# Optimization experiments

Hardware: AMD Instinct MI355X
Metric: run time of the kernel (lower is better)

Reference implementation:

```python
import jax, jax.numpy as jnp
import numpy as np

HIDDEN = 300
INPUT_DIM = 300


def setup_inputs() -> dict:
    key = jax.random.key(0)
    k_in, k_wih, k_whh, k_bih, k_bhh = jax.random.split(key, 5)
    bound = 1.0 / np.sqrt(HIDDEN)  # PyTorch RNNCell init: U(-1/sqrt(H), 1/sqrt(H))
    inputs = jax.random.normal(k_in, (512, 512, INPUT_DIM), dtype=jnp.float32)
    W_ih = jax.random.uniform(k_wih, (HIDDEN, INPUT_DIM), jnp.float32, -bound, bound)
    W_hh = jax.random.uniform(k_whh, (HIDDEN, HIDDEN), jnp.float32, -bound, bound)
    b_ih = jax.random.uniform(k_bih, (HIDDEN,), jnp.float32, -bound, bound)
    b_hh = jax.random.uniform(k_bhh, (HIDDEN,), jnp.float32, -bound, bound)
    return {"inputs": inputs, "W_ih": W_ih, "W_hh": W_hh, "b_ih": b_ih, "b_hh": b_hh}


def reference(inputs, W_ih, W_hh, b_ih, b_hh):
    # inputs: [seq, batch, input_dim]; vanilla tanh RNNCell scanned over time.
    seq, bz, _ = inputs.shape
    # Precompute input projections for all timesteps in one big GEMM.
    x_proj = jnp.einsum('sbi,hi->sbh', inputs, W_ih) + b_ih + b_hh  # [seq, batch, H]

    def step(ht, xp):
        ht = jnp.tanh(xp + ht @ W_hh.T)
        return ht, None

    h0 = jnp.zeros((bz, HIDDEN), dtype=inputs.dtype)
    ht, _ = jax.lax.scan(step, h0, x_proj)
    return ht
```

## Files before the change

### kernel.cpp

```cpp
#include <hip/hip_runtime.h>
#include <hip/hip_bf16.h>


typedef unsigned short u16;
typedef unsigned int   u32;
typedef __attribute__((ext_vector_type(8)))  short bf16x8;
typedef __attribute__((ext_vector_type(4)))  short s16x4;
typedef __attribute__((ext_vector_type(4)))  float f32x4;
typedef __attribute__((ext_vector_type(16))) float f32x16;
typedef __attribute__((ext_vector_type(2)))  unsigned int u32x2;
typedef __attribute__((ext_vector_type(4)))  unsigned int u32x4;

#define HID 300
#define KP  320
#define SEQ 512
#define BZ  512
#define MTOT (SEQ*BZ)

__device__ __forceinline__ u16 f2bf(float f) {
    u32 u = __float_as_uint(f);
    return (u16)((u + 0x7FFFu + ((u >> 16) & 1u)) >> 16);
}
__device__ __forceinline__ float bf2f(u16 h) {
    return __uint_as_float((u32)h << 16);
}
__device__ __forceinline__ float tanh_fast(float x) {
    float e = __builtin_amdgcn_exp2f(x * 2.8853900817779268f);
    float r = __builtin_amdgcn_rcpf(e + 1.0f);
    return __builtin_fmaf(-2.0f, r, 1.0f);
}
__device__ __forceinline__ u32 pack2(float a, float b) {
    __hip_bfloat162 t = __float22bfloat162_rn(float2{a, b});
    return *(u32*)&t;
}
__device__ __forceinline__ void lds_barrier() {
    asm volatile("s_waitcnt lgkmcnt(0)\n\ts_barrier" ::: "memory");
}

__global__ void prep_kernel(const float* __restrict__ wih,
                            const float* __restrict__ whh,
                            const float* __restrict__ bih,
                            const float* __restrict__ bhh,
                            u16* __restrict__ wihp, u16* __restrict__ whhp,
                            float* __restrict__ bias) {
    int n = blockIdx.x, k = threadIdx.x;
    bool v = (n < HID) && (k < HID);
    int src = n * HID + k, dst = n * KP + k;
    wihp[dst] = v ? f2bf(wih[src]) : (u16)0;
    whhp[dst] = v ? f2bf(whh[src]) : (u16)0;
    if (k == 0) bias[n] = (n < HID) ? (bih[n] + bhh[n]) : 0.0f;
}

__global__ __launch_bounds__(512, 1) void xproj_kernel(
    const float* __restrict__ in, const u16* __restrict__ wihp,
    const float* __restrict__ bias, u16* __restrict__ xp) {
    __shared__ __align__(16) u16 As[2][4096];
    __shared__ __align__(16) u16 Bs[3][10240];

    const int tid = threadIdx.x;
    const int w = tid >> 6, l = tid & 63;
    const int mi = w & 3, ni = w >> 2;
    const int l31 = l & 31, l5 = l >> 5;
    const int m0 = blockIdx.x * 128;

    const int sm = tid >> 2, skg = tid & 3;

    f32x16 acc[5];
#pragma unroll
    for (int j = 0; j < 5; ++j)
#pragma unroll
        for (int r = 0; r < 16; ++r) acc[j][r] = 0.0f;

    const f32x4 zf = {0.f, 0.f, 0.f, 0.f};
    auto loadA = [&](int it, f32x4& v0, f32x4& v1) {
        int gk = it * 32 + skg * 8;
        int a0 = gk > 296 ? 296 : gk;
        int a1 = (gk + 4) > 296 ? 296 : (gk + 4);
        const float* p = in + (size_t)(m0 + sm) * HID;
        v0 = *(const f32x4*)(p + a0);
        v1 = *(const f32x4*)(p + a1);
        v0 = (gk > 296) ? zf : v0;
        v1 = ((gk + 4) > 296) ? zf : v1;
    };
    auto writeA = [&](int buf, const f32x4& v0, const f32x4& v1) {
        u32x4 pk;
        pk[0] = pack2(v0[0], v0[1]); pk[1] = pack2(v0[2], v0[3]);
        pk[2] = pack2(v1[0], v1[1]); pk[3] = pack2(v1[2], v1[3]);
        *(u32x4*)&As[buf][(skg >> 1) * 2048 + sm * 16 + (skg & 1) * 8] = pk;
    };
    auto stageB = [&](int buf, int it) {
#pragma unroll
        for (int s = 0; s < 3; ++s) {
            int i = w + 8 * s;
            if (i < 20) {
                int c = i & 3, ng = i >> 2;
                int n = ng * 64 + l;
                const u16* g = wihp + n * KP + it * 32 + c * 8;
                u16* d = &Bs[buf][c * 2560 + ng * 512];
                __builtin_amdgcn_global_load_lds(
                    (const __attribute__((address_space(1))) void*)g,
                    (__attribute__((address_space(3))) void*)d, 16, 0, 0);
            }
        }
    };

    {
        stageB(0, 0);
        f32x4 v0, v1;
        loadA(0, v0, v1);
        writeA(0, v0, v1);
        stageB(1, 1);
        asm volatile("s_waitcnt vmcnt(2)" ::: "memory");
        lds_barrier();
    }

    int cA = 0, cB = 0, sB = 2;
#pragma unroll 1
    for (int it = 0; it < 10; ++it) {
        f32x4 v0, v1;
        if (it < 9) loadA(it + 1, v0, v1);
        if (it < 8) stageB(sB, it + 2);
#pragma unroll
        for (int s = 0; s < 2; ++s) {
            bf16x8 a = *(const bf16x8*)&As[cA][s * 2048 + mi * 512 + l31 * 16 + l5 * 8];
#pragma unroll
            for (int j = 0; j < 5; ++j) {
                bf16x8 b = *(const bf16x8*)&Bs[cB][(s * 2 + l5) * 2560 + ((ni * 5 + j) * 32 + l31) * 8];
                acc[j] = __builtin_amdgcn_mfma_f32_32x32x16_bf16(a, b, acc[j], 0, 0, 0);
            }
        }
        if (it < 9) {
            writeA(cA ^ 1, v0, v1);
            if (it < 8) asm volatile("s_waitcnt vmcnt(3)" ::: "memory");
            else        asm volatile("s_waitcnt vmcnt(2)" ::: "memory");
            lds_barrier();
        }
        cA ^= 1;
        cB = (cB == 2) ? 0 : cB + 1;
        sB = (sB == 2) ? 0 : sB + 1;
    }

    const int mbase = m0 + mi * 32;
#pragma unroll
    for (int j = 0; j < 5; ++j) {
        int n = (ni * 5 + j) * 32 + l31;
        if (n < HID) {
            float bs = bias[n];
#pragma unroll
            for (int reg = 0; reg < 16; ++reg) {
                int row = (reg & 3) + 8 * (reg >> 2) + 4 * l5;
                xp[(size_t)(mbase + row) * HID + n] = f2bf(acc[j][reg] + bs);
            }
        }
    }
}

__global__ __launch_bounds__(512, 2) void rnn_recur_kernel(
    const u16* __restrict__ xp, const u16* __restrict__ whhp,
    float* __restrict__ out) {
    __shared__ __align__(16) u16 hb[2][16 * 328];

    const int tid = threadIdx.x;
    const int w = tid >> 6;
    const int l = tid & 63;
    const int br = l & 15;
    const int q  = l >> 4;
    const int b0 = blockIdx.x * 16;
    const bool t3 = (w < 4);

    for (int i = tid; i < (2 * 16 * 328) / 2; i += 512) ((u32*)hb)[i] = 0;

    bf16x8 Af[3][10];
#pragma unroll
    for (int j = 0; j < 3; ++j) {
        if (j < 2 || t3) {
            const int nt = w + 8 * j;
            const u16* wrow = whhp + (size_t)(nt * 16 + br) * KP;
#pragma unroll
            for (int ks = 0; ks < 10; ++ks)
                Af[j][ks] = *(const bf16x8*)(wrow + ks * 32 + q * 8);
        }
    }
#pragma unroll
    for (int j = 0; j < 3; ++j)
        if (j < 2 || t3)
#pragma unroll
            for (int ks = 0; ks < 10; ++ks)
                asm volatile("" : "+a"(Af[j][ks]));

    int xo[3];
#pragma unroll
    for (int j = 0; j < 3; ++j) {
        int n0 = (w + 8 * j) * 16 + q * 4;
        xo[j] = (n0 < HID && (j < 2 || t3)) ? ((b0 + br) * HID + n0) : -1;
    }

    const s16x4 z4 = {0, 0, 0, 0};
    s16x4 xc[3], xn[3];
#pragma unroll
    for (int j = 0; j < 3; ++j) {
        xc[j] = (xo[j] >= 0) ? *(const s16x4*)(xp + xo[j]) : z4;
        xn[j] = (xo[j] >= 0) ? *(const s16x4*)(xp + (size_t)BZ * HID + xo[j]) : z4;
    }

    lds_barrier();

#pragma unroll 1
    for (int t = 0; t < SEQ; ++t) {
        const u16* hc = hb[t & 1];
        u16*       hn = hb[(t + 1) & 1];

        s16x4 xf[3];
        {
            int t2 = (t + 2 < SEQ) ? (t + 2) : (SEQ - 1);
            const u16* base = xp + (size_t)t2 * (BZ * HID);
#pragma unroll
            for (int j = 0; j < 3; ++j)
                xf[j] = (xo[j] >= 0) ? *(const s16x4*)(base + xo[j]) : z4;
        }

        bf16x8 bL[5];
#pragma unroll
        for (int ks = 0; ks < 5; ++ks)
            bL[ks] = *(const bf16x8*)&hc[br * 328 + ks * 32 + q * 8];

        f32x4 a0L, a1L, a2L;
#pragma unroll
        for (int r = 0; r < 4; ++r) {
            a0L[r] = bf2f((u16)xc[0][r]);
            a1L[r] = bf2f((u16)xc[1][r]);
            a2L[r] = bf2f((u16)xc[2][r]);
        }
#pragma unroll
        for (int ks = 0; ks < 5; ++ks) {
            a0L = __builtin_amdgcn_mfma_f32_16x16x32_bf16(Af[0][ks], bL[ks], a0L, 0, 0, 0);
            a1L = __builtin_amdgcn_mfma_f32_16x16x32_bf16(Af[1][ks], bL[ks], a1L, 0, 0, 0);
            if (t3)
                a2L = __builtin_amdgcn_mfma_f32_16x16x32_bf16(Af[2][ks], bL[ks], a2L, 0, 0, 0);
        }

        bf16x8 bH[5];
#pragma unroll
        for (int ks = 0; ks < 5; ++ks)
            bH[ks] = *(const bf16x8*)&hc[br * 328 + (ks + 5) * 32 + q * 8];

        f32x4 a0H, a1H, a2H;
#pragma unroll
        for (int r = 0; r < 4; ++r) { a0H[r] = 0.f; a1H[r] = 0.f; a2H[r] = 0.f; }

#pragma unroll
        for (int ks = 0; ks < 5; ++ks)
            a0H = __builtin_amdgcn_mfma_f32_16x16x32_bf16(Af[0][ks + 5], bH[ks], a0H, 0, 0, 0);
        {
            int n0 = w * 16 + q * 4;
            u32x2 pk;
            pk[0] = pack2(tanh_fast(a0L[0] + a0H[0]), tanh_fast(a0L[1] + a0H[1]));
            pk[1] = pack2(tanh_fast(a0L[2] + a0H[2]), tanh_fast(a0L[3] + a0H[3]));
            *(u32x2*)&hn[br * 328 + n0] = pk;
        }

#pragma unroll
        for (int ks = 0; ks < 5; ++ks)
            a1H = __builtin_amdgcn_mfma_f32_16x16x32_bf16(Af[1][ks + 5], bH[ks], a1H, 0, 0, 0);
        {
            int n0 = (w + 8) * 16 + q * 4;
            u32x2 pk;
            pk[0] = pack2(tanh_fast(a1L[0] + a1H[0]), tanh_fast(a1L[1] + a1H[1]));
            pk[1] = pack2(tanh_fast(a1L[2] + a1H[2]), tanh_fast(a1L[3] + a1H[3]));
            *(u32x2*)&hn[br * 328 + n0] = pk;
        }

        if (t3) {
#pragma unroll
            for (int ks = 0; ks < 5; ++ks)
                a2H = __builtin_amdgcn_mfma_f32_16x16x32_bf16(Af[2][ks + 5], bH[ks], a2H, 0, 0, 0);
            int n0 = (w + 16) * 16 + q * 4;
            u32x2 pk;
            pk[0] = pack2(tanh_fast(a2L[0] + a2H[0]), tanh_fast(a2L[1] + a2H[1]));
            pk[1] = pack2(tanh_fast(a2L[2] + a2H[2]), tanh_fast(a2L[3] + a2H[3]));
            *(u32x2*)&hn[br * 328 + n0] = pk;
        }

        lds_barrier();

#pragma unroll
        for (int j = 0; j < 3; ++j) { xc[j] = xn[j]; xn[j] = xf[j]; }
    }

    const u16* hf = hb[0];
    for (int i = tid; i < 16 * HID; i += 512) {
        int r = i / HID, n = i - r * HID;
        out[(size_t)(b0 + r) * HID + n] = bf2f(hf[r * 328 + n]);
    }
}

extern "C" void kernel_launch(void* const* d_in, const int* in_sizes, int n_in,
                              void* d_out, int out_size, void* d_ws, size_t ws_size,
                              hipStream_t stream) {
    const float* in  = (const float*)d_in[0];
    const float* wih = (const float*)d_in[1];
    const float* whh = (const float*)d_in[2];
    const float* bih = (const float*)d_in[3];
    const float* bhh = (const float*)d_in[4];

    char* ws = (char*)d_ws;
    const size_t XP_BYTES = (size_t)MTOT * HID * sizeof(u16);
    u16*   xpb  = (u16*)ws;
    u16*   wihp = (u16*)(ws + XP_BYTES);
    u16*   whhp = (u16*)(ws + XP_BYTES + (size_t)KP * KP * 2);
    float* bias = (float*)(ws + XP_BYTES + 2 * (size_t)KP * KP * 2);

    prep_kernel<<<KP, KP, 0, stream>>>(wih, whh, bih, bhh, wihp, whhp, bias);
    xproj_kernel<<<MTOT / 128, 512, 0, stream>>>(in, wihp, bias, xpb);
    rnn_recur_kernel<<<BZ / 16, 512, 0, stream>>>(xpb, whhp, (float*)d_out);
}
```

Baseline: 1.258 ms.

## Split recurrent step into K-halves to overlap tanh writeback with next-step MFMAs

The RNN recurrence now uses a single LDS hidden-state buffer. Each step is split into two phases around two barriers. The low-K half of h (columns below 160) is written first, so the next step's low-half MFMAs can start while the high-half tanh results are still being stored. Two accumulator sets alternate across an unrolled pair of steps, and the first step skips the high-half matmul. The goal is to shorten the serial dependency chain per timestep, at the cost of a second barrier per step and more accumulator registers.

```diff
diff --git a/kernel.cpp b/kernel.cpp
--- a/kernel.cpp
+++ b/kernel.cpp
@@ -158,7 +158,7 @@
 __global__ __launch_bounds__(512, 2) void rnn_recur_kernel(
     const u16* __restrict__ xp, const u16* __restrict__ whhp,
     float* __restrict__ out) {
-    __shared__ __align__(16) u16 hb[2][16 * 328];
+    __shared__ __align__(16) u16 hb[16 * 328];
 
     const int tid = threadIdx.x;
     const int w = tid >> 6;
@@ -167,8 +167,7 @@
     const int q  = l >> 4;
     const int b0 = blockIdx.x * 16;
     const bool t3 = (w < 4);
-
-    for (int i = tid; i < (2 * 16 * 328) / 2; i += 512) ((u32*)hb)[i] = 0;
+    const bool j1low = (w < 2);
 
     bf16x8 Af[3][10];
 #pragma unroll
@@ -203,94 +202,101 @@
         xn[j] = (xo[j] >= 0) ? *(const s16x4*)(xp + (size_t)BZ * HID + xo[j]) : z4;
     }
 
-    lds_barrier();
-
-#pragma unroll 1
-    for (int t = 0; t < SEQ; ++t) {
-        const u16* hc = hb[t & 1];
-        u16*       hn = hb[(t + 1) & 1];
+    f32x4 aP[3], aQ[3];
+#pragma unroll
+    for (int j = 0; j < 3; ++j)
+#pragma unroll
+        for (int r = 0; r < 4; ++r) {
+            aP[j][r] = bf2f((u16)xc[j][r]);
+            aQ[j][r] = 0.0f;
+        }
+
+    auto stepf = [&](f32x4* aC, f32x4* aN, int t) {
+        if (t > 0) {
+            bf16x8 bH[5];
+#pragma unroll
+            for (int ks = 0; ks < 5; ++ks)
+                bH[ks] = *(const bf16x8*)&hb[br * 328 + (ks + 5) * 32 + q * 8];
+#pragma unroll
+            for (int ks = 0; ks < 5; ++ks) {
+                aC[0] = __builtin_amdgcn_mfma_f32_16x16x32_bf16(Af[0][ks + 5], bH[ks], aC[0], 0, 0, 0);
+                aC[1] = __builtin_amdgcn_mfma_f32_16x16x32_bf16(Af[1][ks + 5], bH[ks], aC[1], 0, 0, 0);
+                if (t3)
+                    aC[2] = __builtin_amdgcn_mfma_f32_16x16x32_bf16(Af[2][ks + 5], bH[ks], aC[2], 0, 0, 0);
+            }
+        }
+        {
+            int n0 = w * 16 + q * 4;
+            u32x2 pk;
+            pk[0] = pack2(tanh_fast(aC[0][0]), tanh_fast(aC[0][1]));
+            pk[1] = pack2(tanh_fast(aC[0][2]), tanh_fast(aC[0][3]));
+            *(u32x2*)&hb[br * 328 + n0] = pk;
+        }
+        if (j1low) {
+            int n0 = (w + 8) * 16 + q * 4;
+            u32x2 pk;
+            pk[0] = pack2(tanh_fast(aC[1][0]), tanh_fast(aC[1][1]));
+            pk[1] = pack2(tanh_fast(aC[1][2]), tanh_fast(aC[1][3]));
+            *(u32x2*)&hb[br * 328 + n0] = pk;
+        }
+        lds_barrier();
+
+        bf16x8 bL[5];
+#pragma unroll
+        for (int ks = 0; ks < 5; ++ks)
+            bL[ks] = *(const bf16x8*)&hb[br * 328 + ks * 32 + q * 8];
 
         s16x4 xf[3];
         {
             int t2 = (t + 2 < SEQ) ? (t + 2) : (SEQ - 1);
-            const u16* base = xp + (size_t)t2 * (BZ * HID);
+            const u16* basef = xp + (size_t)t2 * (BZ * HID);
 #pragma unroll
             for (int j = 0; j < 3; ++j)
-                xf[j] = (xo[j] >= 0) ? *(const s16x4*)(base + xo[j]) : z4;
-        }
-
-        bf16x8 bL[5];
-#pragma unroll
-        for (int ks = 0; ks < 5; ++ks)
-            bL[ks] = *(const bf16x8*)&hc[br * 328 + ks * 32 + q * 8];
-
-        f32x4 a0L, a1L, a2L;
-#pragma unroll
-        for (int r = 0; r < 4; ++r) {
-            a0L[r] = bf2f((u16)xc[0][r]);
-            a1L[r] = bf2f((u16)xc[1][r]);
-            a2L[r] = bf2f((u16)xc[2][r]);
-        }
-#pragma unroll
-        for (int ks = 0; ks < 5; ++ks) {
-            a0L = __builtin_amdgcn_mfma_f32_16x16x32_bf16(Af[0][ks], bL[ks], a0L, 0, 0, 0);
-            a1L = __builtin_amdgcn_mfma_f32_16x16x32_bf16(Af[1][ks], bL[ks], a1L, 0, 0, 0);
-            if (t3)
-                a2L = __builtin_amdgcn_mfma_f32_16x16x32_bf16(Af[2][ks], bL[ks], a2L, 0, 0, 0);
-        }
-
-        bf16x8 bH[5];
-#pragma unroll
-        for (int ks = 0; ks < 5; ++ks)
-            bH[ks] = *(const bf16x8*)&hc[br * 328 + (ks + 5) * 32 + q * 8];
-
-        f32x4 a0H, a1H, a2H;
-#pragma unroll
-        for (int r = 0; r < 4; ++r) { a0H[r] = 0.f; a1H[r] = 0.f; a2H[r] = 0.f; }
-
-#pragma unroll
-        for (int ks = 0; ks < 5; ++ks)
-            a0H = __builtin_amdgcn_mfma_f32_16x16x32_bf16(Af[0][ks + 5], bH[ks], a0H, 0, 0, 0);
-        {
-            int n0 = w * 16 + q * 4;
-            u32x2 pk;
-            pk[0] = pack2(tanh_fast(a0L[0] + a0H[0]), tanh_fast(a0L[1] + a0H[1]));
-            pk[1] = pack2(tanh_fast(a0L[2] + a0H[2]), tanh_fast(a0L[3] + a0H[3]));
-            *(u32x2*)&hn[br * 328 + n0] = pk;
-        }
-
-#pragma unroll
-        for (int ks = 0; ks < 5; ++ks)
-            a1H = __builtin_amdgcn_mfma_f32_16x16x32_bf16(Af[1][ks + 5], bH[ks], a1H, 0, 0, 0);
-        {
+                xf[j] = (xo[j] >= 0) ? *(const s16x4*)(basef + xo[j]) : z4;
+        }
+
+        if (!j1low) {
             int n0 = (w + 8) * 16 + q * 4;
             u32x2 pk;
-            pk[0] = pack2(tanh_fast(a1L[0] + a1H[0]), tanh_fast(a1L[1] + a1H[1]));
-            pk[1] = pack2(tanh_fast(a1L[2] + a1H[2]), tanh_fast(a1L[3] + a1H[3]));
-            *(u32x2*)&hn[br * 328 + n0] = pk;
-        }
-
+            pk[0] = pack2(tanh_fast(aC[1][0]), tanh_fast(aC[1][1]));
+            pk[1] = pack2(tanh_fast(aC[1][2]), tanh_fast(aC[1][3]));
+            *(u32x2*)&hb[br * 328 + n0] = pk;
+        }
         if (t3) {
-#pragma unroll
-            for (int ks = 0; ks < 5; ++ks)
-                a2H = __builtin_amdgcn_mfma_f32_16x16x32_bf16(Af[2][ks + 5], bH[ks], a2H, 0, 0, 0);
             int n0 = (w + 16) * 16 + q * 4;
             u32x2 pk;
-            pk[0] = pack2(tanh_fast(a2L[0] + a2H[0]), tanh_fast(a2L[1] + a2H[1]));
-            pk[1] = pack2(tanh_fast(a2L[2] + a2H[2]), tanh_fast(a2L[3] + a2H[3]));
-            *(u32x2*)&hn[br * 328 + n0] = pk;
-        }
-
+            pk[0] = pack2(tanh_fast(aC[2][0]), tanh_fast(aC[2][1]));
+            pk[1] = pack2(tanh_fast(aC[2][2]), tanh_fast(aC[2][3]));
+            *(u32x2*)&hb[br * 328 + n0] = pk;
+        }
+
+#pragma unroll
+        for (int j = 0; j < 3; ++j)
+#pragma unroll
+            for (int r = 0; r < 4; ++r)
+                aN[j][r] = bf2f((u16)xn[j][r]);
+#pragma unroll
+        for (int ks = 0; ks < 5; ++ks) {
+            aN[0] = __builtin_amdgcn_mfma_f32_16x16x32_bf16(Af[0][ks], bL[ks], aN[0], 0, 0, 0);
+            aN[1] = __builtin_amdgcn_mfma_f32_16x16x32_bf16(Af[1][ks], bL[ks], aN[1], 0, 0, 0);
+            if (t3)
+                aN[2] = __builtin_amdgcn_mfma_f32_16x16x32_bf16(Af[2][ks], bL[ks], aN[2], 0, 0, 0);
+        }
+
+#pragma unroll
+        for (int j = 0; j < 3; ++j) { xc[j] = xn[j]; xn[j] = xf[j]; }
         lds_barrier();
-
-#pragma unroll
-        for (int j = 0; j < 3; ++j) { xc[j] = xn[j]; xn[j] = xf[j]; }
-    }
-
-    const u16* hf = hb[0];
+    };
+
+#pragma unroll 1
+    for (int t = 0; t < SEQ; t += 2) {
+        stepf(aP, aQ, t);
+        stepf(aQ, aP, t + 1);
+    }
+
     for (int i = tid; i < 16 * HID; i += 512) {
         int r = i / HID, n = i - r * HID;
-        out[(size_t)(b0 + r) * HID + n] = bf2f(hf[r * 328 + n]);
+        out[(size_t)(b0 + r) * HID + n] = bf2f(hb[r * 328 + n]);
     }
 }
 
```

Measured after the change: 1.389 ms. 1.1x slower.
